# Kernel optimization log

Hardware: AMD Instinct MI355X
Metric: run time of the kernel (lower is better)

Reference implementation:

```python
import jax, jax.numpy as jnp
import numpy as np

NUM_HEADS = 16
NUM_KV_HEADS = 8
HEAD_DIM = 128
EPS = 1e-6
SLIDING_WINDOW = 1024
ROPE_THETA = 10000.0


def _rms_norm(x, w):
    # per-head RMSNorm in fp32, as in Qwen3RMSNorm
    xf = x.astype(jnp.float32)
    var = jnp.mean(xf * xf, axis=-1, keepdims=True)
    return (w * (xf * jax.lax.rsqrt(var + EPS))).astype(x.dtype)


def _rotate_half(x):
    d = x.shape[-1] // 2
    return jnp.concatenate([-x[..., d:], x[..., :d]], axis=-1)


def setup_inputs() -> dict:
    key = jax.random.key(0)
    ks = jax.random.split(key, 6)
    B, S, H = 2, 2048, 2048
    hidden_states = jax.random.normal(ks[0], (B, S, H), dtype=jnp.float32)
    # RoPE tables per HF convention: cos/sin of shape [B, S, head_dim]
    inv_freq = 1.0 / (ROPE_THETA ** (np.arange(0, HEAD_DIM, 2, dtype=np.float32) / HEAD_DIM))
    pos = np.arange(S, dtype=np.float32)
    ang = np.outer(pos, inv_freq)  # [S, HEAD_DIM/2]
    emb = np.concatenate([ang, ang], axis=-1)  # [S, HEAD_DIM]
    cos = jnp.broadcast_to(jnp.asarray(np.cos(emb)), (B, S, HEAD_DIM))
    sin = jnp.broadcast_to(jnp.asarray(np.sin(emb)), (B, S, HEAD_DIM))
    sc = 0.02
    Wq = jax.random.normal(ks[1], (NUM_HEADS * HEAD_DIM, H), dtype=jnp.float32) * sc
    Wk = jax.random.normal(ks[2], (NUM_KV_HEADS * HEAD_DIM, H), dtype=jnp.float32) * sc
    Wv = jax.random.normal(ks[3], (NUM_KV_HEADS * HEAD_DIM, H), dtype=jnp.float32) * sc
    Wo = jax.random.normal(ks[4], (H, NUM_HEADS * HEAD_DIM), dtype=jnp.float32) * sc
    q_norm_w = jnp.ones((HEAD_DIM,), dtype=jnp.float32)
    k_norm_w = jnp.ones((HEAD_DIM,), dtype=jnp.float32)
    return {"hidden_states": hidden_states, "cos": cos, "sin": sin,
            "Wq": Wq, "Wk": Wk, "Wv": Wv, "Wo": Wo,
            "q_norm_w": q_norm_w, "k_norm_w": k_norm_w}


def reference(hidden_states, cos, sin, Wq, Wk, Wv, Wo, q_norm_w, k_norm_w):
    B, S, H = hidden_states.shape
    scaling = HEAD_DIM ** -0.5
    # projections (torch Linear: y = x @ W.T), reshape to [B, nH, S, D]
    q = jnp.einsum('bsh,oh->bso', hidden_states, Wq).reshape(B, S, NUM_HEADS, HEAD_DIM)
    k = jnp.einsum('bsh,oh->bso', hidden_states, Wk).reshape(B, S, NUM_KV_HEADS, HEAD_DIM)
    v = jnp.einsum('bsh,oh->bso', hidden_states, Wv).reshape(B, S, NUM_KV_HEADS, HEAD_DIM)
    q = _rms_norm(q, q_norm_w).transpose(0, 2, 1, 3)  # [B, nH, S, D]
    k = _rms_norm(k, k_norm_w).transpose(0, 2, 1, 3)  # [B, nKV, S, D]
    v = v.transpose(0, 2, 1, 3)
    # RoPE, cos/sin broadcast over heads (unsqueeze_dim=1)
    c = cos[:, None, :, :]
    s = sin[:, None, :, :]
    q = q * c + _rotate_half(q) * s
    k = k * c + _rotate_half(k) * s
    # GQA: repeat kv heads
    groups = NUM_HEADS // NUM_KV_HEADS
    k = jnp.repeat(k, groups, axis=1)
    v = jnp.repeat(v, groups, axis=1)
    # causal + sliding-window mask
    i = jnp.arange(S)[:, None]
    j = jnp.arange(S)[None, :]
    mask = (j <= i) & (i - j < SLIDING_WINDOW)  # [S, S]
    scores = jnp.einsum('bhqd,bhkd->bhqk', q, k) * scaling
    scores = jnp.where(mask[None, None], scores, jnp.finfo(scores.dtype).min)
    probs = jax.nn.softmax(scores, axis=-1)
    attn = jnp.einsum('bhqk,bhkd->bhqd', probs, v)  # [B, nH, S, D]
    attn = attn.transpose(0, 2, 1, 3).reshape(B, S, NUM_HEADS * HEAD_DIM)
    out = jnp.einsum('bso,ho->bsh', attn, Wo)
    return out
```

## Files before the change

### kernel.cpp

```cpp
#include <hip/hip_runtime.h>
#include <stdint.h>

#define S_LEN 2048
#define BATCH 2
#define HID 2048
#define NH 16
#define NKV 8
#define HD 128
#define WINDOW 1024
#define SCALE 0.08838834764831845f
#define QKVW 4096

typedef unsigned short u16;
typedef unsigned int u32;
typedef __attribute__((ext_vector_type(8))) short short8;
typedef __attribute__((ext_vector_type(4))) float f32x4;
typedef __attribute__((ext_vector_type(16))) float f32x16;
typedef __attribute__((ext_vector_type(4))) u16 u16x4;

__device__ __forceinline__ u16 f2b(float f) {
  u32 u = __builtin_bit_cast(u32, f);
  return (u16)((u + 0x7fffu + ((u >> 16) & 1u)) >> 16);
}
__device__ __forceinline__ float b2f(u16 h) {
  u32 u = ((u32)h) << 16;
  return __builtin_bit_cast(float, u);
}
__device__ __forceinline__ u32 pk_bf16(float a, float b) {
  u32 d;
  asm("v_cvt_pk_bf16_f32 %0, %1, %2" : "=v"(d) : "v"(a), "v"(b));
  return d;
}

__device__ __forceinline__ void gload_lds16(const u16* g, u16* l) {
  __builtin_amdgcn_global_load_lds(
      (const __attribute__((address_space(1))) u32*)g,
      (__attribute__((address_space(3))) u32*)l, 16, 0, 0);
}

template <int N>
__device__ __forceinline__ void wait_vm() {
  if constexpr (N == 0) asm volatile("s_waitcnt vmcnt(0)" ::: "memory");
}

#define CQ0 2097152
#define CQ1 3145728
#define CQ2 3670016
#define CQ3 4194304
#define CQ4 5242880
__global__ __launch_bounds__(256) void k_conv5(const float* __restrict__ s0,
                                               const float* __restrict__ s1,
                                               const float* __restrict__ s2,
                                               const float* __restrict__ s3,
                                               const float* __restrict__ s4,
                                               u16* __restrict__ dst) {
  int i = blockIdx.x * blockDim.x + threadIdx.x;
  const int st = gridDim.x * blockDim.x;
  for (; i < CQ4; i += st) {
    const f32x4* src;
    if (i < CQ0)      src = (const f32x4*)s0 + i;
    else if (i < CQ1) src = (const f32x4*)s1 + (i - CQ0);
    else if (i < CQ2) src = (const f32x4*)s2 + (i - CQ1);
    else if (i < CQ3) src = (const f32x4*)s3 + (i - CQ2);
    else              src = (const f32x4*)s4 + (i - CQ3);
    f32x4 v = *src;
    u16x4 o;
    o[0] = f2b(v[0]); o[1] = f2b(v[1]); o[2] = f2b(v[2]); o[3] = f2b(v[3]);
    ((u16x4*)dst)[i] = o;
  }
}

__device__ __forceinline__ void store_c(u16* C, long idx, float v) { C[idx] = f2b(v); }
__device__ __forceinline__ void store_c(float* C, long idx, float v) { C[idx] = v; }

template <typename OutT>
__global__ __launch_bounds__(128, 2) void k_gemmV(const u16* __restrict__ A,
                                                  const u16* __restrict__ B,
                                                  OutT* __restrict__ C,
                                                  int M, int N, int K) {
  __shared__ u16 sA[128 * 64];
  __shared__ u16 sB[128 * 64];
  const int tid = threadIdx.x;
  const int lane = tid & 63;
  const int w = tid >> 6;
  const int l15 = lane & 15;
  const int lg = lane >> 4;
  const int sw = l15 & 7;

  const int gx = gridDim.x;
  const int nwg = gx * gridDim.y;
  const int flat = blockIdx.y * gx + blockIdx.x;
  const int tile = (flat & 7) * (nwg >> 3) + (flat >> 3);
  const long m0 = (long)(tile / gx) * 128;
  const long n0 = (long)(tile % gx) * 128;

  const u16* Abase = A + m0 * K;
  const u16* Bbase = B + n0 * K;

  int aOff[8], dstOff[8];
#pragma unroll
  for (int i = 0; i < 8; ++i) {
    const int c = tid + i * 128;
    const int row = c >> 3, chs = c & 7;
    aOff[i] = row * K + (chs ^ (row & 7)) * 8;
    dstOff[i] = c * 8;
  }

  f32x4 acc[8][4];
  const f32x4 z4 = {0.f, 0.f, 0.f, 0.f};
#pragma unroll
  for (int i = 0; i < 8; ++i)
#pragma unroll
    for (int j = 0; j < 4; ++j) acc[i][j] = z4;

  const int akc0 = (lg ^ sw) * 8;
  const int akc1 = ((4 + lg) ^ sw) * 8;
  const int brow0 = w * 64;

  const int NT = K >> 6;

  for (int t = 0; t < NT; ++t) {
#pragma unroll
    for (int i = 0; i < 8; ++i)
      gload_lds16(Abase + aOff[i] + t * 64, &sA[dstOff[i]]);
#pragma unroll
    for (int i = 0; i < 8; ++i)
      gload_lds16(Bbase + aOff[i] + t * 64, &sB[dstOff[i]]);
    wait_vm<0>();
    __builtin_amdgcn_sched_barrier(0);
    __builtin_amdgcn_s_barrier();
    __builtin_amdgcn_sched_barrier(0);

#pragma unroll
    for (int kk = 0; kk < 2; ++kk) {
      const int akc = (kk == 0) ? akc0 : akc1;
      short8 afk[8], bfk[4];
#pragma unroll
      for (int i = 0; i < 8; ++i)
        afk[i] = *(const short8*)&sA[(i * 16 + l15) * 64 + akc];
#pragma unroll
      for (int j = 0; j < 4; ++j)
        bfk[j] = *(const short8*)&sB[(brow0 + j * 16 + l15) * 64 + akc];
      __builtin_amdgcn_s_setprio(1);
#pragma unroll
      for (int i = 0; i < 8; ++i)
#pragma unroll
        for (int j = 0; j < 4; ++j)
          acc[i][j] = __builtin_amdgcn_mfma_f32_16x16x32_bf16(
              afk[i], bfk[j], acc[i][j], 0, 0, 0);
      __builtin_amdgcn_s_setprio(0);
    }
    __builtin_amdgcn_s_barrier();
    __builtin_amdgcn_sched_barrier(0);
  }

#pragma unroll
  for (int i = 0; i < 8; ++i)
#pragma unroll
    for (int j = 0; j < 4; ++j)
#pragma unroll
      for (int r = 0; r < 4; ++r) {
        long row = m0 + i * 16 + lg * 4 + r;
        long col = n0 + w * 64 + j * 16 + l15;
        store_c(C, row * (long)N + col, acc[i][j][r]);
      }
}

template <typename OutT>
__global__ __launch_bounds__(256, 4) void k_gemmS(const u16* __restrict__ A,
                                                  const u16* __restrict__ B,
                                                  OutT* __restrict__ C,
                                                  int M, int N, int K) {
  __shared__ u16 sA[128 * 64];
  __shared__ u16 sB[128 * 64];
  const int tid = threadIdx.x;
  const int lane = tid & 63;
  const int w = tid >> 6;
  const int l15 = lane & 15;
  const int lg = lane >> 4;
  const int wm = w >> 1;
  const int wn = w & 1;
  const int sw = l15 & 7;

  const int gx = gridDim.x;
  const int nwg = gx * gridDim.y;
  const int flat = blockIdx.y * gx + blockIdx.x;
  const int tile = (flat & 7) * (nwg >> 3) + (flat >> 3);
  const long m0 = (long)(tile / gx) * 128;
  const long n0 = (long)(tile % gx) * 128;

  const u16* Abase = A + m0 * K;
  const u16* Bbase = B + n0 * K;

  int aOff[4], dstOff[4];
#pragma unroll
  for (int i = 0; i < 4; ++i) {
    const int c = tid + i * 256;
    const int row = c >> 3, chs = c & 7;
    aOff[i] = row * K + (chs ^ (row & 7)) * 8;
    dstOff[i] = c * 8;
  }

  f32x4 acc[4][4];
  const f32x4 z4 = {0.f, 0.f, 0.f, 0.f};
#pragma unroll
  for (int i = 0; i < 4; ++i)
#pragma unroll
    for (int j = 0; j < 4; ++j) acc[i][j] = z4;

  const int arow = (wm * 64 + l15) * 64;
  const int brow = (wn * 64 + l15) * 64;
  const int akc0 = (lg ^ sw) * 8;
  const int akc1 = ((4 + lg) ^ sw) * 8;

  const int NT = K >> 6;

  for (int t = 0; t < NT; ++t) {
#pragma unroll
    for (int i = 0; i < 4; ++i)
      gload_lds16(Abase + aOff[i] + t * 64, &sA[dstOff[i]]);
#pragma unroll
    for (int i = 0; i < 4; ++i)
      gload_lds16(Bbase + aOff[i] + t * 64, &sB[dstOff[i]]);
    wait_vm<0>();
    __builtin_amdgcn_sched_barrier(0);
    __builtin_amdgcn_s_barrier();
    __builtin_amdgcn_sched_barrier(0);

#pragma unroll
    for (int kk = 0; kk < 2; ++kk) {
      const int akc = (kk == 0) ? akc0 : akc1;
      short8 afk[4], bfk[4];
#pragma unroll
      for (int i = 0; i < 4; ++i)
        afk[i] = *(const short8*)&sA[arow + i * 16 * 64 + akc];
#pragma unroll
      for (int j = 0; j < 4; ++j)
        bfk[j] = *(const short8*)&sB[brow + j * 16 * 64 + akc];
      __builtin_amdgcn_s_setprio(1);
#pragma unroll
      for (int i = 0; i < 4; ++i)
#pragma unroll
        for (int j = 0; j < 4; ++j)
          acc[i][j] = __builtin_amdgcn_mfma_f32_16x16x32_bf16(
              afk[i], bfk[j], acc[i][j], 0, 0, 0);
      __builtin_amdgcn_s_setprio(0);
    }
    __builtin_amdgcn_s_barrier();
    __builtin_amdgcn_sched_barrier(0);
  }

#pragma unroll
  for (int i = 0; i < 4; ++i)
#pragma unroll
    for (int j = 0; j < 4; ++j)
#pragma unroll
      for (int r = 0; r < 4; ++r) {
        long row = m0 + wm * 64 + i * 16 + lg * 4 + r;
        long col = n0 + wn * 64 + j * 16 + l15;
        store_c(C, row * (long)N + col, acc[i][j][r]);
      }
}

__global__ __launch_bounds__(256) void k_normrope(u16* __restrict__ QKV,
                                                  const float* __restrict__ cosb,
                                                  const float* __restrict__ sinb,
                                                  const float* __restrict__ qw,
                                                  const float* __restrict__ kw) {
  const int lane = threadIdx.x & 63;
  const int w = threadIdx.x >> 6;
  int row = blockIdx.x * 4 + w;
  const int nQ = BATCH * S_LEN * NH;
  u16* p;
  const float* nw;
  int tok;
  float sc;
  if (row < nQ) {
    tok = row >> 4;
    int h = row & 15;
    p = QKV + (long)tok * QKVW + h * HD;
    nw = qw;
    sc = SCALE;
  } else {
    int r2 = row - nQ;
    tok = r2 >> 3;
    int h = r2 & 7;
    p = QKV + (long)tok * QKVW + 2048 + h * HD;
    nw = kw;
    sc = 1.0f;
  }
  float x0 = b2f(p[lane]);
  float x1 = b2f(p[lane + 64]);
  float ss = x0 * x0 + x1 * x1;
#pragma unroll
  for (int mk = 1; mk < 64; mk <<= 1) ss += __shfl_xor(ss, mk, 64);
  float rinv = rsqrtf(ss * (1.0f / 128.0f) + 1e-6f);
  float y0 = x0 * rinv * nw[lane];
  float y1 = x1 * rinv * nw[lane + 64];
  const float* cp = cosb + (long)tok * HD;
  const float* sp = sinb + (long)tok * HD;
  float o0 = (y0 * cp[lane] - y1 * sp[lane]) * sc;
  float o1 = (y1 * cp[lane + 64] + y0 * sp[lane + 64]) * sc;
  p[lane] = f2b(o0);
  p[lane + 64] = f2b(o1);
}

__global__ __launch_bounds__(256, 2) void k_attn(const u16* __restrict__ QKV,
                                                 u16* __restrict__ AO) {
  __shared__ u16 sK[64 * 128];
  __shared__ u16 sVT[64 * 128];
  const int tid = threadIdx.x;
  const int lane = tid & 63;
  const int l31 = lane & 31;
  const int hi = lane >> 5;
  const int w = tid >> 6;
  const int q0 = blockIdx.x * 128;
  const int h = blockIdx.y;
  const int b = blockIdx.z;
  const int kvh = h >> 1;
  const int qw0 = q0 + w * 32;
  const int iq = qw0 + l31;

  const long tokbase = (long)b * S_LEN;
  const u16* Qrow = QKV + (tokbase + qw0 + l31) * QKVW + h * HD;
  short8 qf[8];
#pragma unroll
  for (int dt = 0; dt < 8; ++dt) qf[dt] = *(const short8*)(Qrow + dt * 16 + hi * 8);

  f32x16 o[4];
#pragma unroll
  for (int n = 0; n < 4; ++n)
#pragma unroll
    for (int r = 0; r < 16; ++r) o[n][r] = 0.f;
  float m = 0.f, lsum = 0.f;

  const u16* Kbase = QKV + tokbase * QKVW + 2048 + kvh * HD;
  const u16* Vbase = QKV + tokbase * QKVW + 3072 + kvh * HD;

  int kc_row[4], kc_off[4];
  u16* kc_dst[4];
#pragma unroll
  for (int i = 0; i < 4; ++i) {
    const int c = tid + 256 * i;
    kc_row[i] = c >> 4;
    kc_off[i] = (((c & 15) ^ ((c >> 4) & 7))) * 8;
    kc_dst[i] = &sK[c * 8];
  }
  const int rp = tid & 31;
  const int dc0 = tid >> 5;
  const int rg_st = rp >> 2;

  int t_lo = q0 - (WINDOW - 1);
  t_lo = (t_lo < 0 ? 0 : t_lo) >> 6;
  const int t_hi = (q0 + 127) >> 6;

  for (int t = t_lo; t <= t_hi; ++t) {
    const int kv0 = t << 6;
#pragma unroll
    for (int i = 0; i < 4; ++i)
      gload_lds16(Kbase + (long)(kv0 + kc_row[i]) * QKVW + kc_off[i], kc_dst[i]);
#pragma unroll
    for (int i = 0; i < 2; ++i) {
      const int dc = dc0 + i * 8;
      const u16* vp = Vbase + (long)(kv0 + 2 * rp) * QKVW + dc * 8;
      short8 v0 = *(const short8*)vp;
      short8 v1 = *(const short8*)(vp + QKVW);
#pragma unroll
      for (int e = 0; e < 8; ++e) {
        const int d = dc * 8 + e;
        const int unit = d * 8 + (rg_st ^ (d & 7));
        ((u32*)sVT)[unit * 4 + (rp & 3)] = (u32)(u16)v0[e] | ((u32)(u16)v1[e] << 16);
      }
    }
    __syncthreads();

    const bool skipw = (kv0 > qw0 + 31) || (kv0 + 63 < qw0 - (WINDOW - 1));
    if (!skipw) {
      const bool full = (kv0 + 63 <= qw0) && ((qw0 + 31) - kv0 < WINDOW);
      f32x16 s0, s1;
#pragma unroll
      for (int r = 0; r < 16; ++r) { s0[r] = 0.f; s1[r] = 0.f; }
      const int rsw = l31 & 7;
#pragma unroll
      for (int dt = 0; dt < 8; ++dt) {
        const int ch = hi + 2 * dt;
        const short8 kf0 = *(const short8*)&sK[(l31 * 16 + (ch ^ rsw)) * 8];
        s0 = __builtin_amdgcn_mfma_f32_32x32x16_bf16(kf0, qf[dt], s0, 0, 0, 0);
        const short8 kf1 = *(const short8*)&sK[((l31 + 32) * 16 + (ch ^ rsw)) * 8];
        s1 = __builtin_amdgcn_mfma_f32_32x32x16_bf16(kf1, qf[dt], s1, 0, 0, 0);
      }
      float p[32];
#pragma unroll
      for (int r = 0; r < 16; ++r) { p[r] = s0[r]; p[16 + r] = s1[r]; }
      if (!full) {
#pragma unroll
        for (int r = 0; r < 32; ++r) {
          const int kk = kv0 + (r >> 4) * 32 + 4 * hi + (r & 3) + 8 * ((r >> 2) & 3);
          p[r] = ((u32)(iq - kk) < (u32)WINDOW) ? p[r] : -3.0e38f;
        }
      }
      float tm = p[0];
#pragma unroll
      for (int r = 1; r < 32; ++r) tm = fmaxf(tm, p[r]);
      tm = fmaxf(tm, __shfl_xor(tm, 32, 64));
      const float mn = fmaxf(m, tm);
      const float al = __expf(m - mn);
      m = mn;
      float rs = 0.f;
#pragma unroll
      for (int r = 0; r < 32; ++r) { p[r] = __expf(p[r] - mn); rs += p[r]; }
      rs += __shfl_xor(rs, 32, 64);
      lsum = lsum * al + rs;
#pragma unroll
      for (int n = 0; n < 4; ++n)
#pragma unroll
        for (int r = 0; r < 16; ++r) o[n][r] *= al;

      short8 pf[4];
#pragma unroll
      for (int ks = 0; ks < 4; ++ks) {
        const int bb = (ks >> 1) * 16 + (ks & 1) * 8;
        u32 a0 = pk_bf16(p[bb + 0], p[bb + 1]);
        u32 b0 = pk_bf16(p[bb + 4], p[bb + 5]);
        u32 a1 = pk_bf16(p[bb + 2], p[bb + 3]);
        u32 b1 = pk_bf16(p[bb + 6], p[bb + 7]);
        asm volatile("v_permlane32_swap_b32 %0, %1" : "+v"(a0), "+v"(b0));
        asm volatile("v_permlane32_swap_b32 %0, %1" : "+v"(a1), "+v"(b1));
        union { u32 u[4]; short8 s; } uu;
        uu.u[0] = a0; uu.u[1] = a1; uu.u[2] = b0; uu.u[3] = b1;
        pf[ks] = uu.s;
      }
#pragma unroll
      for (int dt = 0; dt < 4; ++dt) {
        const int d = l31 + 32 * dt;
        const int dsw = d & 7;
#pragma unroll
        for (int ks = 0; ks < 4; ++ks) {
          const int rg = ks * 2 + hi;
          const short8 vf = *(const short8*)&sVT[(d * 8 + (rg ^ dsw)) * 8];
          o[dt] = __builtin_amdgcn_mfma_f32_32x32x16_bf16(vf, pf[ks], o[dt], 0, 0, 0);
        }
      }
    }
    __syncthreads();
  }

  __syncthreads();
  float* R = ((float*)sK) + w * 1024;
  const float rl = 1.0f / lsum;
  const int half = hi;
#pragma unroll
  for (int dt = 0; dt < 4; ++dt) {
#pragma unroll
    for (int r = 0; r < 16; ++r) {
      const int dp = 4 * hi + (r & 3) + 8 * (r >> 2);
      R[dp * 32 + (l31 ^ (4 * (dp & 7)))] = o[dt][r] * rl;
    }
    __syncthreads();
    union { u16 hh[16]; short8 s[2]; } U;
#pragma unroll
    for (int j = 0; j < 16; ++j) {
      const int dp = half * 16 + j;
      U.hh[j] = f2b(R[dp * 32 + (l31 ^ (4 * (dp & 7)))]);
    }
    u16* dst = AO + (tokbase + q0 + w * 32 + l31) * (NH * HD) + h * HD + dt * 32 + half * 16;
    *(short8*)dst = U.s[0];
    *(short8*)(dst + 8) = U.s[1];
    __syncthreads();
  }
}

extern "C" void kernel_launch(void* const* d_in, const int* in_sizes, int n_in,
                              void* d_out, int out_size, void* d_ws, size_t ws_size,
                              hipStream_t stream) {
  const float* hs   = (const float*)d_in[0];
  const float* cosb = (const float*)d_in[1];
  const float* sinb = (const float*)d_in[2];
  const float* Wq   = (const float*)d_in[3];
  const float* Wk   = (const float*)d_in[4];
  const float* Wv   = (const float*)d_in[5];
  const float* Wo   = (const float*)d_in[6];
  const float* qw   = (const float*)d_in[7];
  const float* kw   = (const float*)d_in[8];
  float* out = (float*)d_out;

  const long SZ_X  = (long)BATCH * S_LEN * HID;
  const long SZ_WQ = (long)NH * HD * HID;
  const long SZ_WK = (long)NKV * HD * HID;
  u16* Xb   = (u16*)d_ws;
  u16* Wqb  = Xb + SZ_X;
  u16* Wkb  = Wqb + SZ_WQ;
  u16* Wvb  = Wkb + SZ_WK;
  u16* Wob  = Wvb + SZ_WK;
  u16* QKVb = Wob + SZ_WQ;
  u16* AOb  = QKVb + (long)BATCH * S_LEN * QKVW;

  k_conv5<<<2048, 256, 0, stream>>>(hs, Wq, Wk, Wv, Wo, Xb);

  k_gemmV<u16><<<dim3(32, 32), 128, 0, stream>>>(
      Xb, Wqb, QKVb, BATCH * S_LEN, QKVW, HID);

  k_normrope<<<(BATCH * S_LEN * (NH + NKV)) / 4, 256, 0, stream>>>(QKVb, cosb, sinb, qw, kw);

  k_attn<<<dim3(S_LEN / 128, NH, BATCH), 256, 0, stream>>>(QKVb, AOb);

  k_gemmS<float><<<dim3(16, 32), 256, 0, stream>>>(
      AOb, Wob, out, BATCH * S_LEN, HID, HID);
}
```

Before: 203.2 us.

## Split-K the output projection, reuse 4-wave GEMM for QKV, lazy softmax rescale

The output projection GEMM now splits K across two blocks per tile and accumulates into a pre-zeroed fp32 output with atomicAdd. This raises the number of workgroups available to fill the GPU. The QKV projection drops the 2-wave 128-thread GEMM and uses the 4-wave 256-thread gemmS kernel. Attention skips the running-max update and the O/lsum rescale unless some lane's new tile max exceeds the current max by more than 8. The costs are an extra zeroing kernel, atomic traffic and nondeterministic summation order in the output, plus exponentials that can reach about e^8 before a rescale.

After: 248.2 us. 1.22x slower.

```diff
diff --git a/kernel.cpp b/kernel.cpp
--- a/kernel.cpp
+++ b/kernel.cpp
@@ -70,101 +70,15 @@
   }
 }
 
+__global__ __launch_bounds__(256) void k_zero(float* __restrict__ p, int n4) {
+  int i = blockIdx.x * blockDim.x + threadIdx.x;
+  const int st = gridDim.x * blockDim.x;
+  const f32x4 z4 = {0.f, 0.f, 0.f, 0.f};
+  for (; i < n4; i += st) ((f32x4*)p)[i] = z4;
+}
+
 __device__ __forceinline__ void store_c(u16* C, long idx, float v) { C[idx] = f2b(v); }
 __device__ __forceinline__ void store_c(float* C, long idx, float v) { C[idx] = v; }
-
-template <typename OutT>
-__global__ __launch_bounds__(128, 2) void k_gemmV(const u16* __restrict__ A,
-                                                  const u16* __restrict__ B,
-                                                  OutT* __restrict__ C,
-                                                  int M, int N, int K) {
-  __shared__ u16 sA[128 * 64];
-  __shared__ u16 sB[128 * 64];
-  const int tid = threadIdx.x;
-  const int lane = tid & 63;
-  const int w = tid >> 6;
-  const int l15 = lane & 15;
-  const int lg = lane >> 4;
-  const int sw = l15 & 7;
-
-  const int gx = gridDim.x;
-  const int nwg = gx * gridDim.y;
-  const int flat = blockIdx.y * gx + blockIdx.x;
-  const int tile = (flat & 7) * (nwg >> 3) + (flat >> 3);
-  const long m0 = (long)(tile / gx) * 128;
-  const long n0 = (long)(tile % gx) * 128;
-
-  const u16* Abase = A + m0 * K;
-  const u16* Bbase = B + n0 * K;
-
-  int aOff[8], dstOff[8];
-#pragma unroll
-  for (int i = 0; i < 8; ++i) {
-    const int c = tid + i * 128;
-    const int row = c >> 3, chs = c & 7;
-    aOff[i] = row * K + (chs ^ (row & 7)) * 8;
-    dstOff[i] = c * 8;
-  }
-
-  f32x4 acc[8][4];
-  const f32x4 z4 = {0.f, 0.f, 0.f, 0.f};
-#pragma unroll
-  for (int i = 0; i < 8; ++i)
-#pragma unroll
-    for (int j = 0; j < 4; ++j) acc[i][j] = z4;
-
-  const int akc0 = (lg ^ sw) * 8;
-  const int akc1 = ((4 + lg) ^ sw) * 8;
-  const int brow0 = w * 64;
-
-  const int NT = K >> 6;
-
-  for (int t = 0; t < NT; ++t) {
-#pragma unroll
-    for (int i = 0; i < 8; ++i)
-      gload_lds16(Abase + aOff[i] + t * 64, &sA[dstOff[i]]);
-#pragma unroll
-    for (int i = 0; i < 8; ++i)
-      gload_lds16(Bbase + aOff[i] + t * 64, &sB[dstOff[i]]);
-    wait_vm<0>();
-    __builtin_amdgcn_sched_barrier(0);
-    __builtin_amdgcn_s_barrier();
-    __builtin_amdgcn_sched_barrier(0);
-
-#pragma unroll
-    for (int kk = 0; kk < 2; ++kk) {
-      const int akc = (kk == 0) ? akc0 : akc1;
-      short8 afk[8], bfk[4];
-#pragma unroll
-      for (int i = 0; i < 8; ++i)
-        afk[i] = *(const short8*)&sA[(i * 16 + l15) * 64 + akc];
-#pragma unroll
-      for (int j = 0; j < 4; ++j)
-        bfk[j] = *(const short8*)&sB[(brow0 + j * 16 + l15) * 64 + akc];
-      __builtin_amdgcn_s_setprio(1);
-#pragma unroll
-      for (int i = 0; i < 8; ++i)
-#pragma unroll
-        for (int j = 0; j < 4; ++j)
-          acc[i][j] = __builtin_amdgcn_mfma_f32_16x16x32_bf16(
-              afk[i], bfk[j], acc[i][j], 0, 0, 0);
-      __builtin_amdgcn_s_setprio(0);
-    }
-    __builtin_amdgcn_s_barrier();
-    __builtin_amdgcn_sched_barrier(0);
-  }
-
-#pragma unroll
-  for (int i = 0; i < 8; ++i)
-#pragma unroll
-    for (int j = 0; j < 4; ++j)
-#pragma unroll
-      for (int r = 0; r < 4; ++r) {
-        long row = m0 + i * 16 + lg * 4 + r;
-        long col = n0 + w * 64 + j * 16 + l15;
-        store_c(C, row * (long)N + col, acc[i][j][r]);
-      }
-}
 
 template <typename OutT>
 __global__ __launch_bounds__(256, 4) void k_gemmS(const u16* __restrict__ A,
@@ -259,6 +173,102 @@
         long row = m0 + wm * 64 + i * 16 + lg * 4 + r;
         long col = n0 + wn * 64 + j * 16 + l15;
         store_c(C, row * (long)N + col, acc[i][j][r]);
+      }
+}
+
+__global__ __launch_bounds__(256, 4) void k_gemmSK(const u16* __restrict__ A,
+                                                   const u16* __restrict__ B,
+                                                   float* __restrict__ C,
+                                                   int M, int N, int K) {
+  __shared__ u16 sA[128 * 64];
+  __shared__ u16 sB[128 * 64];
+  const int tid = threadIdx.x;
+  const int lane = tid & 63;
+  const int w = tid >> 6;
+  const int l15 = lane & 15;
+  const int lg = lane >> 4;
+  const int wm = w >> 1;
+  const int wn = w & 1;
+  const int sw = l15 & 7;
+
+  const int gx = gridDim.x;
+  const int nwg = gx * gridDim.y;
+  const int flat = blockIdx.y * gx + blockIdx.x;
+  const int tile = (flat & 7) * (nwg >> 3) + (flat >> 3);
+  const long m0 = (long)(tile / gx) * 128;
+  const long n0 = (long)(tile % gx) * 128;
+  const int koff = blockIdx.z * (K >> 1);
+
+  const u16* Abase = A + m0 * K + koff;
+  const u16* Bbase = B + n0 * K + koff;
+
+  int aOff[4], dstOff[4];
+#pragma unroll
+  for (int i = 0; i < 4; ++i) {
+    const int c = tid + i * 256;
+    const int row = c >> 3, chs = c & 7;
+    aOff[i] = row * K + (chs ^ (row & 7)) * 8;
+    dstOff[i] = c * 8;
+  }
+
+  f32x4 acc[4][4];
+  const f32x4 z4 = {0.f, 0.f, 0.f, 0.f};
+#pragma unroll
+  for (int i = 0; i < 4; ++i)
+#pragma unroll
+    for (int j = 0; j < 4; ++j) acc[i][j] = z4;
+
+  const int arow = (wm * 64 + l15) * 64;
+  const int brow = (wn * 64 + l15) * 64;
+  const int akc0 = (lg ^ sw) * 8;
+  const int akc1 = ((4 + lg) ^ sw) * 8;
+
+  const int NT = (K >> 1) >> 6;
+
+  for (int t = 0; t < NT; ++t) {
+#pragma unroll
+    for (int i = 0; i < 4; ++i)
+      gload_lds16(Abase + aOff[i] + t * 64, &sA[dstOff[i]]);
+#pragma unroll
+    for (int i = 0; i < 4; ++i)
+      gload_lds16(Bbase + aOff[i] + t * 64, &sB[dstOff[i]]);
+    wait_vm<0>();
+    __builtin_amdgcn_sched_barrier(0);
+    __builtin_amdgcn_s_barrier();
+    __builtin_amdgcn_sched_barrier(0);
+
+#pragma unroll
+    for (int kk = 0; kk < 2; ++kk) {
+      const int akc = (kk == 0) ? akc0 : akc1;
+      short8 afk[4], bfk[4];
+#pragma unroll
+      for (int i = 0; i < 4; ++i)
+        afk[i] = *(const short8*)&sA[arow + i * 16 * 64 + akc];
+#pragma unroll
+      for (int j = 0; j < 4; ++j)
+        bfk[j] = *(const short8*)&sB[brow + j * 16 * 64 + akc];
+      __builtin_amdgcn_s_setprio(1);
+#pragma unroll
+      for (int i = 0; i < 4; ++i)
+#pragma unroll
+        for (int j = 0; j < 4; ++j)
+          acc[i][j] = __builtin_amdgcn_mfma_f32_16x16x32_bf16(
+              afk[i], bfk[j], acc[i][j], 0, 0, 0);
+      __builtin_amdgcn_s_setprio(0);
+    }
+    __builtin_amdgcn_s_barrier();
+    __builtin_amdgcn_sched_barrier(0);
+  }
+
+#pragma unroll
+  for (int i = 0; i < 4; ++i)
+#pragma unroll
+    for (int j = 0; j < 4; ++j)
+#pragma unroll
+      for (int r = 0; r < 4; ++r) {
+        long row = m0 + wm * 64 + i * 16 + lg * 4 + r;
+        long col = n0 + wn * 64 + j * 16 + l15;
+        atomicAdd(&C[row * (long)N + col], acc[i][j][r]);
       }
 }
 
@@ -403,18 +413,21 @@
 #pragma unroll
       for (int r = 1; r < 32; ++r) tm = fmaxf(tm, p[r]);
       tm = fmaxf(tm, __shfl_xor(tm, 32, 64));
-      const float mn = fmaxf(m, tm);
-      const float al = __expf(m - mn);
-      m = mn;
+      if (!__all(tm - m <= 8.0f)) {
+        const float mn = fmaxf(m, tm);
+        const float al = __expf(m - mn);
+        m = mn;
+        lsum *= al;
+#pragma unroll
+        for (int n = 0; n < 4; ++n)
+#pragma unroll
+          for (int r = 0; r < 16; ++r) o[n][r] *= al;
+      }
       float rs = 0.f;
 #pragma unroll
-      for (int r = 0; r < 32; ++r) { p[r] = __expf(p[r] - mn); rs += p[r]; }
+      for (int r = 0; r < 32; ++r) { p[r] = __expf(p[r] - m); rs += p[r]; }
       rs += __shfl_xor(rs, 32, 64);
-      lsum = lsum * al + rs;
-#pragma unroll
-      for (int n = 0; n < 4; ++n)
-#pragma unroll
-        for (int r = 0; r < 16; ++r) o[n][r] *= al;
+      lsum += rs;
 
       short8 pf[4];
 #pragma unroll
@@ -463,7 +476,7 @@
       const int dp = half * 16 + j;
       U.hh[j] = f2b(R[dp * 32 + (l31 ^ (4 * (dp & 7)))]);
     }
-    u16* dst = AO + (tokbase + q0 + w * 32 + l31) * (NH * HD) + h * HD + dt * 32 + half * 16;
+    u16* dst = AO + (tokbase + qw0 + l31) * (NH * HD) + h * HD + dt * 32 + half * 16;
     *(short8*)dst = U.s[0];
     *(short8*)(dst + 8) = U.s[1];
     __syncthreads();
@@ -497,13 +510,15 @@
 
   k_conv5<<<2048, 256, 0, stream>>>(hs, Wq, Wk, Wv, Wo, Xb);
 
-  k_gemmV<u16><<<dim3(32, 32), 128, 0, stream>>>(
+  k_gemmS<u16><<<dim3(32, 32), 256, 0, stream>>>(
       Xb, Wqb, QKVb, BATCH * S_LEN, QKVW, HID);
 
-  k_normrope<<<(BATCH * S_LEN * (NH + NKV)) / 4, 256, 0, stream>>>(QKVb, cosb, sinb, qw, kw);
+  k_normrope<<<(BATCH * S_LEN * (NH + NKV)) / 4, 256, 0, stream>>>(
+      QKVb, cosb, sinb, qw, kw);
 
   k_attn<<<dim3(S_LEN / 128, NH, BATCH), 256, 0, stream>>>(QKVb, AOb);
 
-  k_gemmS<float><<<dim3(16, 32), 256, 0, stream>>>(
+  k_zero<<<2048, 256, 0, stream>>>(out, (int)((long)BATCH * S_LEN * HID / 4));
+  k_gemmSK<<<dim3(16, 32, 2), 256, 0, stream>>>(
       AOb, Wob, out, BATCH * S_LEN, HID, HID);
 }
```
